# Optimization experiments

Measured on AMD Instinct MI355X. Metric: run time of the kernel, lower is better.

The kernel has to match this reference:

```python
import jax, jax.numpy as jnp
import numpy as np

TOP_K = 2
B, S, H, I, E = 1, 2048, 1024, 4096, 8


def setup_inputs() -> dict:
    key = jax.random.key(0)
    k1, k2, k3, k4 = jax.random.split(key, 4)
    x = jax.random.normal(k1, (B, S, H), dtype=jnp.float32)
    gate_w = jax.random.normal(k2, (E, H), dtype=jnp.float32)
    w1 = jax.random.normal(k3, (E, I, H), dtype=jnp.float32)
    w2 = jax.random.normal(k4, (E, H, I), dtype=jnp.float32)
    return {"x": x, "gate_w": gate_w, "w1": w1, "w2": w2}


def reference(x, gate_w, w1, w2):
    b, s, h = x.shape
    xf = x.reshape(-1, h)                      # [T, H]
    T = xf.shape[0]
    logits = xf @ gate_w.T                     # [T, E]
    probs = jax.nn.softmax(logits, axis=-1)
    wts, idx = jax.lax.top_k(probs, TOP_K)     # [T, k]
    wts = wts / jnp.sum(wts, axis=-1, keepdims=True)
    # combine[t, e] = routing weight of expert e for token t (0 if not selected)
    combine = jnp.zeros((T, w1.shape[0]), dtype=x.dtype)
    combine = combine.at[jnp.arange(T)[:, None], idx].add(wts)
    # dense dispatch: every expert processes every token, masked/weighted by combine
    hid = jax.nn.silu(jnp.einsum('th,eih->tei', xf, w1))   # [T, E, I]
    y = jnp.einsum('tei,ehi->teh', hid, w2)                # [T, E, H]
    out = jnp.einsum('teh,te->th', y, combine)             # [T, H]
    return out.reshape(b, s, h)
```

## Files before the change

### kernel.cpp

```cpp
#include <hip/hip_runtime.h>
#include <stdint.h>

#define TT 2048
#define HH 1024
#define II 4096
#define EE 8

typedef __attribute__((ext_vector_type(4))) float floatx4;
typedef __attribute__((ext_vector_type(8))) __bf16 bf16x8;

__device__ __forceinline__ unsigned short f2bf(float f) {
  union { float f; unsigned u; } v; v.f = f;
  return (unsigned short)((v.u + 0x7FFFu + ((v.u >> 16) & 1u)) >> 16);
}

__device__ __forceinline__ void async_ld16(const void* g, void* l) {
  __builtin_amdgcn_global_load_lds(
      (__attribute__((address_space(1))) void*)g,
      (__attribute__((address_space(3))) void*)l, 16, 0, 0);
}

__global__ __launch_bounds__(256) void k_gating(
    const float* __restrict__ x, const float* __restrict__ gw,
    unsigned short* __restrict__ xb, int* __restrict__ sel_e,
    float* __restrict__ sel_w, int* __restrict__ counts) {
  int t = blockIdx.x;
  int tid = threadIdx.x;
  floatx4 xv = ((const floatx4*)(x + (size_t)t * HH))[tid];
  ushort4 xo;
  xo.x = f2bf(xv.x); xo.y = f2bf(xv.y); xo.z = f2bf(xv.z); xo.w = f2bf(xv.w);
  ((ushort4*)(xb + (size_t)t * HH))[tid] = xo;

  float part[EE];
#pragma unroll
  for (int e = 0; e < EE; e++) {
    floatx4 g = ((const floatx4*)(gw + e * HH))[tid];
    part[e] = xv.x * g.x + xv.y * g.y + xv.z * g.z + xv.w * g.w;
  }
#pragma unroll
  for (int e = 0; e < EE; e++) {
    float v = part[e];
#pragma unroll
    for (int off = 32; off > 0; off >>= 1) v += __shfl_down(v, off, 64);
    part[e] = v;
  }
  __shared__ float red[4][EE];
  int wave = tid >> 6;
  if ((tid & 63) == 0) {
#pragma unroll
    for (int e = 0; e < EE; e++) red[wave][e] = part[e];
  }
  __syncthreads();
  if (tid == 0) {
    float lg[EE];
#pragma unroll
    for (int e = 0; e < EE; e++)
      lg[e] = red[0][e] + red[1][e] + red[2][e] + red[3][e];
    int e0 = 0;
#pragma unroll
    for (int e = 1; e < EE; e++) if (lg[e] > lg[e0]) e0 = e;
    int e1 = (e0 == 0) ? 1 : 0;
#pragma unroll
    for (int e = 0; e < EE; e++) if (e != e0 && lg[e] > lg[e1]) e1 = e;
    float w0 = 1.f / (1.f + expf(lg[e1] - lg[e0]));
    sel_e[t * 2] = e0; sel_e[t * 2 + 1] = e1;
    sel_w[t * 2] = w0; sel_w[t * 2 + 1] = 1.f - w0;
    atomicAdd(&counts[e0], 1);
    atomicAdd(&counts[e1], 1);
  }
}

__global__ void k_scan(const int* __restrict__ counts, int* __restrict__ bases) {
  if (threadIdx.x == 0 && blockIdx.x == 0) {
    int s = 0;
    for (int e = 0; e < EE; e++) { bases[e] = s; s += counts[e]; }
  }
}

__global__ __launch_bounds__(256) void k_fill(
    const int* __restrict__ sel_e, const float* __restrict__ sel_w,
    const int* __restrict__ bases, int* __restrict__ cnt2,
    int* __restrict__ row_token, float* __restrict__ row_w) {
  int p = blockIdx.x * 256 + threadIdx.x;
  if (p >= TT * 2) return;
  int e = sel_e[p];
  int slot = bases[e] + atomicAdd(&cnt2[e], 1);
  row_token[slot] = p >> 1;
  row_w[slot] = sel_w[p];
}

__global__ __launch_bounds__(256) void k_convert(
    const float* __restrict__ w1, const float* __restrict__ w2,
    unsigned short* __restrict__ w1b, unsigned short* __restrict__ w2b) {
  const size_t N1 = (size_t)EE * II * HH;
  size_t i = ((size_t)blockIdx.x * 256 + threadIdx.x) * 4;
  const size_t stride = (size_t)gridDim.x * 256 * 4;
  for (; i < 2 * N1; i += stride) {
    const float* s; unsigned short* d; size_t j;
    if (i < N1) { s = w1; d = w1b; j = i; } else { s = w2; d = w2b; j = i - N1; }
    floatx4 v = *(const floatx4*)(s + j);
    ushort4 o;
    o.x = f2bf(v.x); o.y = f2bf(v.y); o.z = f2bf(v.z); o.w = f2bf(v.w);
    *(ushort4*)(d + j) = o;
  }
}

__global__ __launch_bounds__(256) void k_gemm1(
    const unsigned short* __restrict__ xb,
    const unsigned short* __restrict__ w1b,
    unsigned short* __restrict__ hid,
    const int* __restrict__ counts, const int* __restrict__ bases,
    const int* __restrict__ row_token) {
  const int e = blockIdx.z;
  const int count = counts[e];
  const int m0 = blockIdx.y * 128;
  if (m0 >= count) return;
  const int n0 = blockIdx.x * 128;
  const int base = bases[e];

  __shared__ __align__(16) unsigned short As[128 * 32];
  __shared__ __align__(16) unsigned short Bs[128 * 32];

  const int tid = threadIdx.x;
  const int lane = tid & 63;
  const int wave = tid >> 6;
  const int wm = (wave & 1) * 64;
  const int wn = (wave >> 1) * 64;
  const int quad = lane >> 4;
  const int l16 = lane & 15;

  const int rA0 = tid >> 2;
  const int rA1 = rA0 + 64;
  const int cc = (tid & 3) * 8;

  int g0 = m0 + rA0; if (g0 > count - 1) g0 = count - 1;
  int g1 = m0 + rA1; if (g1 > count - 1) g1 = count - 1;
  const unsigned short* aS0 = xb + (size_t)row_token[base + g0] * HH + cc;
  const unsigned short* aS1 = xb + (size_t)row_token[base + g1] * HH + cc;
  const unsigned short* wp = w1b + (size_t)e * II * HH;
  const unsigned short* bS0 = wp + (size_t)(n0 + rA0) * HH + cc;
  const unsigned short* bS1 = wp + (size_t)(n0 + rA1) * HH + cc;

  unsigned short* lA0 = As + tid * 8;
  unsigned short* lA1 = As + tid * 8 + 2048;
  unsigned short* lB0 = Bs + tid * 8;
  unsigned short* lB1 = Bs + tid * 8 + 2048;

  const floatx4 fz = {0.f, 0.f, 0.f, 0.f};
  floatx4 acc[4][4];
#pragma unroll
  for (int i = 0; i < 4; i++)
#pragma unroll
    for (int j = 0; j < 4; j++) acc[i][j] = fz;

  for (int k0 = 0; k0 < HH; k0 += 32) {
    async_ld16(aS0 + k0, lA0);
    async_ld16(aS1 + k0, lA1);
    async_ld16(bS0 + k0, lB0);
    async_ld16(bS1 + k0, lB1);
    __syncthreads();
    bf16x8 af[4], bfr[4];
#pragma unroll
    for (int i = 0; i < 4; i++) {
      af[i]  = *(const bf16x8*)(As + (wm + i * 16 + l16) * 32 + quad * 8);
      bfr[i] = *(const bf16x8*)(Bs + (wn + i * 16 + l16) * 32 + quad * 8);
    }
#pragma unroll
    for (int i = 0; i < 4; i++)
#pragma unroll
      for (int j = 0; j < 4; j++)
        acc[i][j] = __builtin_amdgcn_mfma_f32_16x16x32_bf16(af[i], bfr[j], acc[i][j], 0, 0, 0);
    __syncthreads();
  }

#pragma unroll
  for (int i = 0; i < 4; i++) {
#pragma unroll
    for (int r = 0; r < 4; r++) {
      const int m = wm + i * 16 + quad * 4 + r;
      if (m0 + m < count) {
        unsigned short* hp = hid + (size_t)(base + m0 + m) * II + n0 + wn + l16;
#pragma unroll
        for (int j = 0; j < 4; j++) {
          float z = acc[i][j][r];
          float s = z / (1.f + __expf(-z));
          hp[j * 16] = f2bf(s);
        }
      }
    }
  }
}

__global__ __launch_bounds__(256) void k_gemm2(
    const unsigned short* __restrict__ hid,
    const unsigned short* __restrict__ w2b,
    float* __restrict__ out,
    const int* __restrict__ counts, const int* __restrict__ bases,
    const int* __restrict__ row_token, const float* __restrict__ row_w) {
  const int e = blockIdx.z;
  const int count = counts[e];
  const int m0 = blockIdx.y * 128;
  if (m0 >= count) return;
  const int nt = blockIdx.x & 7;
  const int ks = blockIdx.x >> 3;
  const int n0 = nt * 128;
  const int base = bases[e];

  __shared__ __align__(16) unsigned short As[128 * 32];
  __shared__ __align__(16) unsigned short Bs[128 * 32];

  const int tid = threadIdx.x;
  const int lane = tid & 63;
  const int wave = tid >> 6;
  const int wm = (wave & 1) * 64;
  const int wn = (wave >> 1) * 64;
  const int quad = lane >> 4;
  const int l16 = lane & 15;

  const int rA0 = tid >> 2;
  const int rA1 = rA0 + 64;
  const int cc = (tid & 3) * 8;

  int g0 = m0 + rA0; if (g0 > count - 1) g0 = count - 1;
  int g1 = m0 + rA1; if (g1 > count - 1) g1 = count - 1;
  const unsigned short* aS0 = hid + (size_t)(base + g0) * II + cc;
  const unsigned short* aS1 = hid + (size_t)(base + g1) * II + cc;
  const unsigned short* wp = w2b + (size_t)e * HH * II;
  const unsigned short* bS0 = wp + (size_t)(n0 + rA0) * II + cc;
  const unsigned short* bS1 = wp + (size_t)(n0 + rA1) * II + cc;

  unsigned short* lA0 = As + tid * 8;
  unsigned short* lA1 = As + tid * 8 + 2048;
  unsigned short* lB0 = Bs + tid * 8;
  unsigned short* lB1 = Bs + tid * 8 + 2048;

  const floatx4 fz = {0.f, 0.f, 0.f, 0.f};
  floatx4 acc[4][4];
#pragma unroll
  for (int i = 0; i < 4; i++)
#pragma unroll
    for (int j = 0; j < 4; j++) acc[i][j] = fz;

  const int kbeg = ks * (II / 2);
  const int kend = kbeg + II / 2;
  for (int k0 = kbeg; k0 < kend; k0 += 32) {
    async_ld16(aS0 + k0, lA0);
    async_ld16(aS1 + k0, lA1);
    async_ld16(bS0 + k0, lB0);
    async_ld16(bS1 + k0, lB1);
    __syncthreads();
    bf16x8 af[4], bfr[4];
#pragma unroll
    for (int i = 0; i < 4; i++) {
      af[i]  = *(const bf16x8*)(As + (wm + i * 16 + l16) * 32 + quad * 8);
      bfr[i] = *(const bf16x8*)(Bs + (wn + i * 16 + l16) * 32 + quad * 8);
    }
#pragma unroll
    for (int i = 0; i < 4; i++)
#pragma unroll
      for (int j = 0; j < 4; j++)
        acc[i][j] = __builtin_amdgcn_mfma_f32_16x16x32_bf16(af[i], bfr[j], acc[i][j], 0, 0, 0);
    __syncthreads();
  }

#pragma unroll
  for (int i = 0; i < 4; i++) {
#pragma unroll
    for (int r = 0; r < 4; r++) {
      const int m = wm + i * 16 + quad * 4 + r;
      if (m0 + m < count) {
        const int row = base + m0 + m;
        const float wgt = row_w[row];
        float* op = out + (size_t)row_token[row] * HH + n0 + wn + l16;
#pragma unroll
        for (int j = 0; j < 4; j++) atomicAdd(op + j * 16, wgt * acc[i][j][r]);
      }
    }
  }
}

extern "C" void kernel_launch(void* const* d_in, const int* in_sizes, int n_in,
                              void* d_out, int out_size, void* d_ws, size_t ws_size,
                              hipStream_t stream) {
  const float* x  = (const float*)d_in[0];
  const float* gw = (const float*)d_in[1];
  const float* w1 = (const float*)d_in[2];
  const float* w2 = (const float*)d_in[3];
  float* out = (float*)d_out;

  char* ws = (char*)d_ws;
  size_t off = 0;
  auto take = [&](size_t n) -> char* {
    char* p = ws + off;
    off += (n + 255) & ~(size_t)255;
    return p;
  };
  unsigned short* xb  = (unsigned short*)take((size_t)TT * HH * 2);
  unsigned short* w1b = (unsigned short*)take((size_t)EE * II * HH * 2);
  unsigned short* w2b = (unsigned short*)take((size_t)EE * HH * II * 2);
  unsigned short* hid = (unsigned short*)take((size_t)TT * 2 * II * 2);
  int*   counts    = (int*)take(EE * 4);
  int*   cnt2      = (int*)take(EE * 4);
  int*   bases     = (int*)take(EE * 4);
  int*   row_token = (int*)take((size_t)TT * 2 * 4);
  float* row_w     = (float*)take((size_t)TT * 2 * 4);
  int*   sel_e     = (int*)take((size_t)TT * 2 * 4);
  float* sel_w     = (float*)take((size_t)TT * 2 * 4);
  if (off > ws_size) return;

  hipMemsetAsync(counts, 0, 512, stream);
  hipMemsetAsync(out, 0, (size_t)TT * HH * 4, stream);

  k_gating<<<TT, 256, 0, stream>>>(x, gw, xb, sel_e, sel_w, counts);
  k_scan<<<1, 64, 0, stream>>>(counts, bases);
  k_fill<<<(TT * 2) / 256, 256, 0, stream>>>(sel_e, sel_w, bases, cnt2, row_token, row_w);
  k_convert<<<8192, 256, 0, stream>>>(w1, w2, w1b, w2b);
  k_gemm1<<<dim3(II / 128, 16, EE), 256, 0, stream>>>(xb, w1b, hid, counts, bases, row_token);
  k_gemm2<<<dim3(16, 16, EE), 256, 0, stream>>>(hid, w2b, out, counts, bases, row_token, row_w);
}
```

Before: 513.5 us.

## Replace atomic scatter with split-K partial buffer and combine, merge scan/fill, widen stores

Several changes land together. k_scan and the old k_fill become one single-block fill kernel that keeps its counters in LDS and records an inverse slot map. k_convert now handles 8 floats per thread and writes 16-byte stores. GEMM1 stages its SiLU epilogue through LDS so it can write hid rows as 16-byte vectors, and both GEMMs get launch_bounds occupancy hints. GEMM2 drops its fp32 atomicAdd scatter and the output memset; it writes split-K partials into the reused w1b buffer, and a new combine kernel gathers and weights them per token. This removes atomic contention at the cost of an extra pass over roughly 32MB of partials.

```diff
diff --git a/kernel.cpp b/kernel.cpp
--- a/kernel.cpp
+++ b/kernel.cpp
@@ -70,42 +70,51 @@
   }
 }
 
-__global__ void k_scan(const int* __restrict__ counts, int* __restrict__ bases) {
-  if (threadIdx.x == 0 && blockIdx.x == 0) {
+__global__ __launch_bounds__(256) void k_fill(
+    const int* __restrict__ counts, const int* __restrict__ sel_e,
+    const float* __restrict__ sel_w, int* __restrict__ bases,
+    int* __restrict__ row_token, float* __restrict__ row_w,
+    int* __restrict__ inv_slot) {
+  __shared__ int lb[EE];
+  __shared__ int lc[EE];
+  int tid = threadIdx.x;
+  if (tid == 0) {
     int s = 0;
-    for (int e = 0; e < EE; e++) { bases[e] = s; s += counts[e]; }
-  }
-}
-
-__global__ __launch_bounds__(256) void k_fill(
-    const int* __restrict__ sel_e, const float* __restrict__ sel_w,
-    const int* __restrict__ bases, int* __restrict__ cnt2,
-    int* __restrict__ row_token, float* __restrict__ row_w) {
-  int p = blockIdx.x * 256 + threadIdx.x;
-  if (p >= TT * 2) return;
-  int e = sel_e[p];
-  int slot = bases[e] + atomicAdd(&cnt2[e], 1);
-  row_token[slot] = p >> 1;
-  row_w[slot] = sel_w[p];
+    for (int e = 0; e < EE; e++) { lb[e] = s; s += counts[e]; }
+  }
+  if (tid < EE) lc[tid] = 0;
+  __syncthreads();
+  for (int p = tid; p < TT * 2; p += 256) {
+    int e = sel_e[p];
+    int slot = lb[e] + atomicAdd(&lc[e], 1);
+    row_token[slot] = p >> 1;
+    row_w[slot] = sel_w[p];
+    inv_slot[p] = slot;
+  }
+  __syncthreads();
+  if (tid < EE) bases[tid] = lb[tid];
 }
 
 __global__ __launch_bounds__(256) void k_convert(
     const float* __restrict__ w1, const float* __restrict__ w2,
     unsigned short* __restrict__ w1b, unsigned short* __restrict__ w2b) {
-  const size_t N1 = (size_t)EE * II * HH;
-  size_t i = ((size_t)blockIdx.x * 256 + threadIdx.x) * 4;
-  const size_t stride = (size_t)gridDim.x * 256 * 4;
-  for (; i < 2 * N1; i += stride) {
-    const float* s; unsigned short* d; size_t j;
-    if (i < N1) { s = w1; d = w1b; j = i; } else { s = w2; d = w2b; j = i - N1; }
-    floatx4 v = *(const floatx4*)(s + j);
-    ushort4 o;
-    o.x = f2bf(v.x); o.y = f2bf(v.y); o.z = f2bf(v.z); o.w = f2bf(v.w);
-    *(ushort4*)(d + j) = o;
-  }
-}
-
-__global__ __launch_bounds__(256) void k_gemm1(
+  const int half_blocks = (int)(((size_t)EE * II * HH) / (256 * 8));
+  const float* s;
+  unsigned short* d;
+  int b = blockIdx.x;
+  if (b < half_blocks) { s = w1; d = w1b; } else { s = w2; d = w2b; b -= half_blocks; }
+  size_t i = ((size_t)b * 256 + threadIdx.x) * 8;
+  floatx4 v0 = *(const floatx4*)(s + i);
+  floatx4 v1 = *(const floatx4*)(s + i + 4);
+  uint4 o;
+  o.x = (unsigned)f2bf(v0.x) | ((unsigned)f2bf(v0.y) << 16);
+  o.y = (unsigned)f2bf(v0.z) | ((unsigned)f2bf(v0.w) << 16);
+  o.z = (unsigned)f2bf(v1.x) | ((unsigned)f2bf(v1.y) << 16);
+  o.w = (unsigned)f2bf(v1.z) | ((unsigned)f2bf(v1.w) << 16);
+  *(uint4*)(d + i) = o;
+}
+
+__global__ __launch_bounds__(256, 3) void k_gemm1(
     const unsigned short* __restrict__ xb,
     const unsigned short* __restrict__ w1b,
     unsigned short* __restrict__ hid,
@@ -118,8 +127,9 @@
   const int n0 = blockIdx.x * 128;
   const int base = bases[e];
 
-  __shared__ __align__(16) unsigned short As[128 * 32];
-  __shared__ __align__(16) unsigned short Bs[128 * 32];
+  __shared__ __align__(16) unsigned short Smem[128 * 32 * 2];
+  unsigned short* As = Smem;
+  unsigned short* Bs = Smem + 128 * 32;
 
   const int tid = threadIdx.x;
   const int lane = tid & 63;
@@ -173,30 +183,35 @@
     __syncthreads();
   }
 
+  unsigned short* Sl = Smem + wave * (16 * 72);
 #pragma unroll
   for (int i = 0; i < 4; i++) {
 #pragma unroll
     for (int r = 0; r < 4; r++) {
-      const int m = wm + i * 16 + quad * 4 + r;
+      const int row16 = quad * 4 + r;
+#pragma unroll
+      for (int j = 0; j < 4; j++) {
+        float z = acc[i][j][r];
+        Sl[row16 * 72 + l16 + 16 * j] = f2bf(z / (1.f + __expf(-z)));
+      }
+    }
+#pragma unroll
+    for (int half = 0; half < 2; half++) {
+      const int row16 = (lane >> 3) + 8 * half;
+      const int m = wm + i * 16 + row16;
       if (m0 + m < count) {
-        unsigned short* hp = hid + (size_t)(base + m0 + m) * II + n0 + wn + l16;
-#pragma unroll
-        for (int j = 0; j < 4; j++) {
-          float z = acc[i][j][r];
-          float s = z / (1.f + __expf(-z));
-          hp[j * 16] = f2bf(s);
-        }
+        bf16x8 v = *(const bf16x8*)(Sl + row16 * 72 + (lane & 7) * 8);
+        *(bf16x8*)(hid + (size_t)(base + m0 + m) * II + n0 + wn + (lane & 7) * 8) = v;
       }
     }
   }
 }
 
-__global__ __launch_bounds__(256) void k_gemm2(
+__global__ __launch_bounds__(256, 3) void k_gemm2(
     const unsigned short* __restrict__ hid,
     const unsigned short* __restrict__ w2b,
-    float* __restrict__ out,
-    const int* __restrict__ counts, const int* __restrict__ bases,
-    const int* __restrict__ row_token, const float* __restrict__ row_w) {
+    float* __restrict__ yp,
+    const int* __restrict__ counts, const int* __restrict__ bases) {
   const int e = blockIdx.z;
   const int count = counts[e];
   const int m0 = blockIdx.y * 128;
@@ -206,8 +221,9 @@
   const int n0 = nt * 128;
   const int base = bases[e];
 
-  __shared__ __align__(16) unsigned short As[128 * 32];
-  __shared__ __align__(16) unsigned short Bs[128 * 32];
+  __shared__ __align__(16) unsigned short Smem2[128 * 32 * 2];
+  unsigned short* As = Smem2;
+  unsigned short* Bs = Smem2 + 128 * 32;
 
   const int tid = threadIdx.x;
   const int lane = tid & 63;
@@ -269,14 +285,29 @@
     for (int r = 0; r < 4; r++) {
       const int m = wm + i * 16 + quad * 4 + r;
       if (m0 + m < count) {
-        const int row = base + m0 + m;
-        const float wgt = row_w[row];
-        float* op = out + (size_t)row_token[row] * HH + n0 + wn + l16;
-#pragma unroll
-        for (int j = 0; j < 4; j++) atomicAdd(op + j * 16, wgt * acc[i][j][r]);
+        float* op = yp + ((size_t)ks * (TT * 2) + base + m0 + m) * HH + n0 + wn + l16;
+#pragma unroll
+        for (int j = 0; j < 4; j++) op[j * 16] = acc[i][j][r];
       }
     }
   }
+}
+
+__global__ __launch_bounds__(256) void k_combine(
+    const float* __restrict__ yp, const int* __restrict__ inv_slot,
+    const float* __restrict__ sel_w, float* __restrict__ out) {
+  const int t = blockIdx.x;
+  const int tid = threadIdx.x;
+  const int s0 = inv_slot[2 * t];
+  const int s1 = inv_slot[2 * t + 1];
+  const float w0 = sel_w[2 * t];
+  const float w1 = sel_w[2 * t + 1];
+  const floatx4 a0 = ((const floatx4*)(yp + (size_t)s0 * HH))[tid];
+  const floatx4 a1 = ((const floatx4*)(yp + ((size_t)(TT * 2) + s0) * HH))[tid];
+  const floatx4 b0 = ((const floatx4*)(yp + (size_t)s1 * HH))[tid];
+  const floatx4 b1 = ((const floatx4*)(yp + ((size_t)(TT * 2) + s1) * HH))[tid];
+  floatx4 v = w0 * (a0 + a1) + w1 * (b0 + b1);
+  ((floatx4*)(out + (size_t)t * HH))[tid] = v;
 }
 
 extern "C" void kernel_launch(void* const* d_in, const int* in_sizes, int n_in,
@@ -300,21 +331,25 @@
   unsigned short* w2b = (unsigned short*)take((size_t)EE * HH * II * 2);
   unsigned short* hid = (unsigned short*)take((size_t)TT * 2 * II * 2);
   int*   counts    = (int*)take(EE * 4);
-  int*   cnt2      = (int*)take(EE * 4);
   int*   bases     = (int*)take(EE * 4);
   int*   row_token = (int*)take((size_t)TT * 2 * 4);
   float* row_w     = (float*)take((size_t)TT * 2 * 4);
   int*   sel_e     = (int*)take((size_t)TT * 2 * 4);
   float* sel_w     = (float*)take((size_t)TT * 2 * 4);
+  int*   inv_slot  = (int*)take((size_t)TT * 2 * 4);
   if (off > ws_size) return;
 
-  hipMemsetAsync(counts, 0, 512, stream);
-  hipMemsetAsync(out, 0, (size_t)TT * HH * 4, stream);
+  float* yp = (float*)w1b;
+
+  hipMemsetAsync(counts, 0, EE * 4, stream);
 
   k_gating<<<TT, 256, 0, stream>>>(x, gw, xb, sel_e, sel_w, counts);
-  k_scan<<<1, 64, 0, stream>>>(counts, bases);
-  k_fill<<<(TT * 2) / 256, 256, 0, stream>>>(sel_e, sel_w, bases, cnt2, row_token, row_w);
-  k_convert<<<8192, 256, 0, stream>>>(w1, w2, w1b, w2b);
+  k_fill<<<1, 256, 0, stream>>>(counts, sel_e, sel_w, bases, row_token, row_w, inv_slot);
+  {
+    const int half_blocks = (int)(((size_t)EE * II * HH) / (256 * 8));
+    k_convert<<<2 * half_blocks, 256, 0, stream>>>(w1, w2, w1b, w2b);
+  }
   k_gemm1<<<dim3(II / 128, 16, EE), 256, 0, stream>>>(xb, w1b, hid, counts, bases, row_token);
-  k_gemm2<<<dim3(16, 16, EE), 256, 0, stream>>>(hid, w2b, out, counts, bases, row_token, row_w);
-}
+  k_gemm2<<<dim3(16, 16, EE), 256, 0, stream>>>(hid, w2b, yp, counts, bases);
+  k_combine<<<TT, 256, 0, stream>>>(yp, inv_slot, sel_w, out);
+}
```

After: 517.1 us. No clear change (+0.7%).
